# Optimization experiments

Measured on AMD Instinct MI355X. Metric: run time of the kernel, lower is better.

## Reference

```python
import jax, jax.numpy as jnp
from jax import lax
import numpy as np

B, T, H = 8192, 1024, 10


def setup_inputs() -> dict:
    key = jax.random.key(0)
    ks = jax.random.split(key, 7)
    s = 1.0 / np.sqrt(H)  # PyTorch default init scale for LSTM/Linear
    return {
        "x": jax.random.normal(ks[0], (B, T, 1), dtype=jnp.float32),
        "W_ih": jax.random.uniform(ks[1], (4 * H, 1), jnp.float32, -s, s),
        "W_hh": jax.random.uniform(ks[2], (4 * H, H), jnp.float32, -s, s),
        "b_ih": jax.random.uniform(ks[3], (4 * H,), jnp.float32, -s, s),
        "b_hh": jax.random.uniform(ks[4], (4 * H,), jnp.float32, -s, s),
        "W_lin": jax.random.uniform(ks[5], (1, H), jnp.float32, -s, s),
        "b_lin": jax.random.uniform(ks[6], (1,), jnp.float32, -s, s),
    }


def reference(x, W_ih, W_hh, b_ih, b_hh, W_lin, b_lin):
    # x: [B, T, 1] (batch_first). PyTorch gate order: i, f, g, o.
    b = b_ih + b_hh  # [4H]
    # Precompute input projections for all timesteps: [T, B, 4H]
    xg = jnp.einsum("bti,gi->tbg", x, W_ih) + b

    def step(carry, xg_t):
        h, c = carry  # each [B, H]
        gates = xg_t + h @ W_hh.T  # [B, 4H]
        i, f, g, o = jnp.split(gates, 4, axis=-1)
        c = jax.nn.sigmoid(f) * c + jax.nn.sigmoid(i) * jnp.tanh(g)
        h = jax.nn.sigmoid(o) * jnpp_tanh(c) if False else jax.nn.sigmoid(o) * jnp.tanh(c)
        return (h, c), None

    h0 = jnp.zeros((x.shape[0], W_hh.shape[1]), x.dtype)
    (_, cT), _ = lax.scan(step, (h0, h0), xg)
    # Module uses the final CELL state c_n, reshaped to [B, H], then Linear(10,1)
    return cT @ W_lin.T + b_lin  # [B, 1]
```

## Files before the change

kernel.cpp:

```cpp
#include <hip/hip_runtime.h>

#define B_TOT 8192
#define T_LEN 1024
#define HID 10

typedef float v2f __attribute__((ext_vector_type(2)));

__global__ __launch_bounds__(256) void lstm_fused_kernel(
    const float* __restrict__ x,
    const float* __restrict__ W_ih,
    const float* __restrict__ W_hh,
    const float* __restrict__ b_ih,
    const float* __restrict__ b_hh,
    const float* __restrict__ W_lin,
    const float* __restrict__ b_lin,
    float* __restrict__ out)
{
    const int tid  = threadIdx.x;
    const int j16  = tid & 15;
    const int b    = blockIdx.x * 16 + (tid >> 4);
    const bool act = (j16 < HID);
    const int j    = act ? j16 : 0;

    v2f w01[HID], w23[HID];
    v2f wi01, wi23, b01, b23;
    {
        const int r0 = 0 * HID + j, r1 = 1 * HID + j;
        const int r2 = 2 * HID + j, r3 = 3 * HID + j;
        wi01 = (v2f){W_ih[r0], W_ih[r1]};
        wi23 = (v2f){W_ih[r2], W_ih[r3]};
        b01  = (v2f){b_ih[r0] + b_hh[r0], b_ih[r1] + b_hh[r1]};
        b23  = (v2f){b_ih[r2] + b_hh[r2], b_ih[r3] + b_hh[r3]};
#pragma unroll
        for (int k = 0; k < HID; ++k) {
            w01[k] = (v2f){W_hh[r0 * HID + k], W_hh[r1 * HID + k]};
            w23[k] = (v2f){W_hh[r2 * HID + k], W_hh[r3 * HID + k]};
        }
    }
    const float wl = act ? W_lin[j] : 0.0f;

    float h = 0.0f, c = 0.0f;
    const float* xb = x + (size_t)b * T_LEN;

    const float LOG2E  = 1.442695040888963f;
    const float LOG2E2 = 2.885390081777927f;
    const v2f mneg = (v2f){-LOG2E, -LOG2E};
    const v2f mgo  = (v2f){LOG2E2, -LOG2E};

#define LSTM_STEP(xv)                                                          \
    {                                                                          \
        v2f xv2 = (v2f){(xv), (xv)};                                           \
        v2f a01 = __builtin_elementwise_fma(xv2, wi01, b01);                   \
        v2f a23 = __builtin_elementwise_fma(xv2, wi23, b23);                   \
        _Pragma("unroll")                                                      \
        for (int k = 0; k < HID; ++k) {                                        \
            float hk = __shfl(h, k, 16);                                       \
            v2f hk2 = (v2f){hk, hk};                                           \
            a01 = __builtin_elementwise_fma(w01[k], hk2, a01);                 \
            a23 = __builtin_elementwise_fma(w23[k], hk2, a23);                 \
        }                                                                      \
        v2f m01 = a01 * mneg;                              \
        v2f m23 = a23 * mgo;                               \
        float ei = __builtin_amdgcn_exp2f(m01.x);                              \
        float ef = __builtin_amdgcn_exp2f(m01.y);                              \
        float eg = __builtin_amdgcn_exp2f(m23.x);                              \
        float eo = __builtin_amdgcn_exp2f(m23.y);                              \
        float ig = __builtin_amdgcn_rcpf(1.0f + ei);          \
        float fg = __builtin_amdgcn_rcpf(1.0f + ef);                           \
        float og = __builtin_amdgcn_rcpf(1.0f + eo);                           \
        float rg = __builtin_amdgcn_rcpf(1.0f + eg);                           \
        float gg = fmaf(-2.0f, rg, 1.0f);                        \
        c = fmaf(fg, c, ig * gg);                                              \
        float ec = __builtin_amdgcn_exp2f(c * LOG2E2);                         \
        float tc = fmaf(-2.0f, __builtin_amdgcn_rcpf(1.0f + ec), 1.0f);        \
        h = og * tc;                                                           \
    }

    float4 xq = *reinterpret_cast<const float4*>(xb);
    for (int t = 0; t < T_LEN; t += 4) {
        float4 xn = make_float4(0.f, 0.f, 0.f, 0.f);
        if (t + 4 < T_LEN)
            xn = *reinterpret_cast<const float4*>(xb + t + 4);
        LSTM_STEP(xq.x)
        LSTM_STEP(xq.y)
        LSTM_STEP(xq.z)
        LSTM_STEP(xq.w)
        xq = xn;
    }
#undef LSTM_STEP

    float v = act ? c * wl : 0.0f;
#pragma unroll
    for (int s = 1; s < 16; s <<= 1) v += __shfl_xor(v, s, 16);
    if (j16 == 0) out[b] = v + b_lin[0];
}

extern "C" void kernel_launch(void* const* d_in, const int* in_sizes, int n_in,
                              void* d_out, int out_size, void* d_ws, size_t ws_size,
                              hipStream_t stream) {
    const float* x     = (const float*)d_in[0];
    const float* W_ih  = (const float*)d_in[1];
    const float* W_hh  = (const float*)d_in[2];
    const float* b_ih  = (const float*)d_in[3];
    const float* b_hh  = (const float*)d_in[4];
    const float* W_lin = (const float*)d_in[5];
    const float* b_lin = (const float*)d_in[6];
    float* out = (float*)d_out;

    dim3 grid(B_TOT / 16), block(256);
    hipLaunchKernelGGL(lstm_fused_kernel, grid, block, 0, stream,
                       x, W_ih, W_hh, b_ih, b_hh, W_lin, b_lin, out);
}
```

Measured before the change: 392.8 us.

## Fold exp2 scales into weights, use DPP broadcast, split FMA chains

Pre-scales the LSTM weights and biases by -log2e or 2*log2e so the gate pre-activations feed exp2 directly. The cell state is kept in a scaled domain (C = 2*log2e*c), and the output weight is rescaled to compensate. The per-step __shfl broadcasts of h are replaced with DPP row broadcasts. Each gate's 10-term FMA chain is split into two accumulators to shorten the dependency chain, and the tail iteration is peeled to drop the bounds check. This removes multiplies and ds_bpermute latency from the serial recurrence, at the cost of slightly different float rounding.

```diff
diff --git a/kernel.cpp b/kernel.cpp
--- a/kernel.cpp
+++ b/kernel.cpp
@@ -5,6 +5,11 @@
 #define HID 10
 
 typedef float v2f __attribute__((ext_vector_type(2)));
+
+
+#define BCAST16(v, K)                                                         \
+    __int_as_float(__builtin_amdgcn_update_dpp(                               \
+        __float_as_int(v), __float_as_int(v), 0x150 | (K), 0xF, 0xF, false))
 
 __global__ __launch_bounds__(256) void lstm_fused_kernel(
     const float* __restrict__ x,
@@ -22,74 +27,80 @@
     const bool act = (j16 < HID);
     const int j    = act ? j16 : 0;
 
+    const float NL = -1.4426950408889634f;
+    const float TL =  2.8853900817779268f;
+
     v2f w01[HID], w23[HID];
     v2f wi01, wi23, b01, b23;
     {
         const int r0 = 0 * HID + j, r1 = 1 * HID + j;
         const int r2 = 2 * HID + j, r3 = 3 * HID + j;
-        wi01 = (v2f){W_ih[r0], W_ih[r1]};
-        wi23 = (v2f){W_ih[r2], W_ih[r3]};
-        b01  = (v2f){b_ih[r0] + b_hh[r0], b_ih[r1] + b_hh[r1]};
-        b23  = (v2f){b_ih[r2] + b_hh[r2], b_ih[r3] + b_hh[r3]};
+        wi01 = (v2f){NL * W_ih[r0], NL * W_ih[r1]};
+        wi23 = (v2f){TL * W_ih[r2], NL * W_ih[r3]};
+        b01  = (v2f){NL * (b_ih[r0] + b_hh[r0]), NL * (b_ih[r1] + b_hh[r1])};
+        b23  = (v2f){TL * (b_ih[r2] + b_hh[r2]), NL * (b_ih[r3] + b_hh[r3])};
 #pragma unroll
         for (int k = 0; k < HID; ++k) {
-            w01[k] = (v2f){W_hh[r0 * HID + k], W_hh[r1 * HID + k]};
-            w23[k] = (v2f){W_hh[r2 * HID + k], W_hh[r3 * HID + k]};
+            w01[k] = (v2f){NL * W_hh[r0 * HID + k], NL * W_hh[r1 * HID + k]};
+            w23[k] = (v2f){TL * W_hh[r2 * HID + k], NL * W_hh[r3 * HID + k]};
         }
     }
-    const float wl = act ? W_lin[j] : 0.0f;
+    const float wl = act ? W_lin[j] * 0.34657359027997264f : 0.0f;
 
-    float h = 0.0f, c = 0.0f;
+    float h = 0.0f, C = 0.0f;
     const float* xb = x + (size_t)b * T_LEN;
 
-    const float LOG2E  = 1.442695040888963f;
-    const float LOG2E2 = 2.885390081777927f;
-    const v2f mneg = (v2f){-LOG2E, -LOG2E};
-    const v2f mgo  = (v2f){LOG2E2, -LOG2E};
+#define ACC(K, A01, A23)                                                      \
+    {                                                                         \
+        float hk = BCAST16(h, K);                                             \
+        v2f hk2 = (v2f){hk, hk};                                              \
+        A01 = __builtin_elementwise_fma(w01[K], hk2, A01);                    \
+        A23 = __builtin_elementwise_fma(w23[K], hk2, A23);                    \
+    }
 
-#define LSTM_STEP(xv)                                                          \
-    {                                                                          \
-        v2f xv2 = (v2f){(xv), (xv)};                                           \
-        v2f a01 = __builtin_elementwise_fma(xv2, wi01, b01);                   \
-        v2f a23 = __builtin_elementwise_fma(xv2, wi23, b23);                   \
-        _Pragma("unroll")                                                      \
-        for (int k = 0; k < HID; ++k) {                                        \
-            float hk = __shfl(h, k, 16);                                       \
-            v2f hk2 = (v2f){hk, hk};                                           \
-            a01 = __builtin_elementwise_fma(w01[k], hk2, a01);                 \
-            a23 = __builtin_elementwise_fma(w23[k], hk2, a23);                 \
-        }                                                                      \
-        v2f m01 = a01 * mneg;                              \
-        v2f m23 = a23 * mgo;                               \
-        float ei = __builtin_amdgcn_exp2f(m01.x);                              \
-        float ef = __builtin_amdgcn_exp2f(m01.y);                              \
-        float eg = __builtin_amdgcn_exp2f(m23.x);                              \
-        float eo = __builtin_amdgcn_exp2f(m23.y);                              \
-        float ig = __builtin_amdgcn_rcpf(1.0f + ei);          \
-        float fg = __builtin_amdgcn_rcpf(1.0f + ef);                           \
-        float og = __builtin_amdgcn_rcpf(1.0f + eo);                           \
-        float rg = __builtin_amdgcn_rcpf(1.0f + eg);                           \
-        float gg = fmaf(-2.0f, rg, 1.0f);                        \
-        c = fmaf(fg, c, ig * gg);                                              \
-        float ec = __builtin_amdgcn_exp2f(c * LOG2E2);                         \
-        float tc = fmaf(-2.0f, __builtin_amdgcn_rcpf(1.0f + ec), 1.0f);        \
-        h = og * tc;                                                           \
+#define LSTM_STEP(xv)                                                         \
+    {                                                                         \
+        v2f xv2 = (v2f){(xv), (xv)};                                          \
+        v2f a01 = __builtin_elementwise_fma(xv2, wi01, b01);                  \
+        v2f a23 = __builtin_elementwise_fma(xv2, wi23, b23);                  \
+        v2f s01 = (v2f){0.0f, 0.0f}, s23 = (v2f){0.0f, 0.0f};                 \
+        ACC(0, a01, a23) ACC(1, a01, a23) ACC(2, a01, a23)                    \
+        ACC(3, a01, a23) ACC(4, a01, a23)                                     \
+        ACC(5, s01, s23) ACC(6, s01, s23) ACC(7, s01, s23)                    \
+        ACC(8, s01, s23) ACC(9, s01, s23)                                     \
+        a01 += s01;                                                           \
+        a23 += s23;                                                           \
+        float ig = __builtin_amdgcn_rcpf(1.0f + __builtin_amdgcn_exp2f(a01.x)); \
+        float fg = __builtin_amdgcn_rcpf(1.0f + __builtin_amdgcn_exp2f(a01.y)); \
+        float rg = __builtin_amdgcn_rcpf(1.0f + __builtin_amdgcn_exp2f(a23.x)); \
+        float og = __builtin_amdgcn_rcpf(1.0f + __builtin_amdgcn_exp2f(a23.y)); \
+        float gg = fmaf(-2.0f * TL, rg, TL);              \
+        C = fmaf(fg, C, ig * gg);                                             \
+        float tc = fmaf(-2.0f,                                                \
+                        __builtin_amdgcn_rcpf(1.0f + __builtin_amdgcn_exp2f(C)), \
+                        1.0f);                                                \
+        h = og * tc;                                                          \
     }
 
     float4 xq = *reinterpret_cast<const float4*>(xb);
-    for (int t = 0; t < T_LEN; t += 4) {
-        float4 xn = make_float4(0.f, 0.f, 0.f, 0.f);
-        if (t + 4 < T_LEN)
-            xn = *reinterpret_cast<const float4*>(xb + t + 4);
+    int t = 0;
+    for (; t < T_LEN - 4; t += 4) {
+        float4 xn = *reinterpret_cast<const float4*>(xb + t + 4);
         LSTM_STEP(xq.x)
         LSTM_STEP(xq.y)
         LSTM_STEP(xq.z)
         LSTM_STEP(xq.w)
         xq = xn;
     }
+    LSTM_STEP(xq.x)
+    LSTM_STEP(xq.y)
+    LSTM_STEP(xq.z)
+    LSTM_STEP(xq.w)
+
 #undef LSTM_STEP
+#undef ACC
 
-    float v = act ? c * wl : 0.0f;
+    float v = act ? C * wl : 0.0f;
 #pragma unroll
     for (int s = 1; s < 16; s <<= 1) v += __shfl_xor(v, s, 16);
     if (j16 == 0) out[b] = v + b_lin[0];
```

New measurement: 356.7 us. -9.2%, faster.
